# Kernel tuning notes

Hardware: AMD Instinct MI355X
Metric: run time of the kernel (lower is better)

## Reference

```python
import jax, jax.numpy as jnp
import numpy as np

V, D, N, E, H = 80000, 300, 32, 64, 4
C = D // H          # per-head out channels (concat -> D)
B, T, U, L = 32, 35, 1024, 3
VG = 50000          # last_idx_globals - last_idx_senses
NEG_SLOPE = 0.2


def setup_inputs() -> dict:
    key = jax.random.key(0)
    ks = jax.random.split(key, 16)
    s = 0.02
    inp = {
        'x_indices': jax.random.randint(ks[0], (B, T, N), 0, V),
        'edge_index': jax.random.randint(ks[1], (B, T, 2, E), 0, N),
        'X': jax.random.normal(ks[2], (V, D), jnp.float32) * s,
        'gat_W': jax.random.normal(ks[3], (D, H * C), jnp.float32) * s,
        'att_src': jax.random.normal(ks[4], (H, C), jnp.float32) * s,
        'att_dst': jax.random.normal(ks[5], (H, C), jnp.float32) * s,
        'gat_bias': jnp.zeros((H * C,), jnp.float32),
        'W_ih0': jax.random.normal(ks[6], (4 * U, 2 * D), jnp.float32) * s,
        'W_ih_rest': jax.random.normal(ks[7], (L - 1, 4 * U, U), jnp.float32) * s,
        'W_hh': jax.random.normal(ks[8], (L, 4 * U, U), jnp.float32) * s,
        'b_ih': jnp.zeros((L, 4 * U), jnp.float32),
        'b_hh': jnp.zeros((L, 4 * U), jnp.float32),
        'lin_W': jax.random.normal(ks[9], (VG, U), jnp.float32) * s,
        'lin_b': jnp.zeros((VG,), jnp.float32),
    }
    return inp


def _gat_node0(X, x_indices, edge_index, gat_W, att_src, att_dst, gat_bias):
    # Batched GATConv over G = B*T tiny subgraphs of fixed size N; dense NxN
    # attention per subgraph is used since N=32 (G*H*N*N ~ 4.6M floats).
    b, t, n = x_indices.shape
    G = b * t
    idx = x_indices.reshape(G, n)
    ei = edge_index.reshape(G, 2, -1)
    x = X[idx]                                   # [G,N,D] embedding gather
    h = (x @ gat_W).reshape(G, n, H, C)          # [G,N,H,C]
    a_s = jnp.einsum('gnhc,hc->gnh', h, att_src)
    a_d = jnp.einsum('gnhc,hc->gnh', h, att_dst)
    # e[g,h,i,j] = leaky_relu(a_dst_i + a_src_j)  (messages j -> i)
    e = a_d.transpose(0, 2, 1)[:, :, :, None] + a_s.transpose(0, 2, 1)[:, :, None, :]
    e = jax.nn.leaky_relu(e, NEG_SLOPE)
    src, dst = ei[:, 0], ei[:, 1]
    g_ar = jnp.arange(G)[:, None]
    adj = jnp.zeros((G, n, n), bool).at[g_ar, dst, src].set(True)
    diag = jnp.arange(n)
    adj = adj.at[:, diag, diag].set(True)        # PyG GATConv adds self-loops
    e = jnp.where(adj[:, None, :, :], e, jnp.float32(-1e9))
    alpha = jax.nn.softmax(e, axis=-1)           # softmax over source nodes j
    out = jnp.einsum('ghij,gjhc->gihc', alpha, h)
    node0 = out[:, 0].reshape(G, H * C) + gat_bias  # only node 0 is consumed
    return node0.reshape(b, t, H * C)


def _lstm_layer(xs, Wi, Wh, bi, bh):
    # xs: [T,B,in]; PyTorch gate order i,f,g,o
    bsz, u = xs.shape[1], Wh.shape[1]
    def step(carry, xt):
        hp, cp = carry
        g = xt @ Wi.T + hp @ Wh.T + (bi + bh)
        i_, f_, gg, o_ = jnp.split(g, 4, axis=-1)
        c = jax.nn.sigmoid(f_) * cp + jax.nn.sigmoid(i_) * jnp.tanh(gg)
        hh = jax.nn.sigmoid(o_) * jnp.tanh(c)
        return (hh, c), hh
    init = (jnp.zeros((bsz, u), xs.dtype), jnp.zeros((bsz, u), xs.dtype))
    _, ys = jax.lax.scan(step, init, xs)
    return ys


def reference(x_indices, edge_index, X, gat_W, att_src, att_dst, gat_bias,
              W_ih0, W_ih_rest, W_hh, b_ih, b_hh, lin_W, lin_b):
    b, t, n = x_indices.shape
    node0 = _gat_node0(X, x_indices, edge_index, gat_W, att_src, att_dst, gat_bias)
    curr_emb = X[x_indices[:, :, 0]]                       # [B,T,D]
    sig = jnp.concatenate([curr_emb, node0], axis=-1)      # [B,T,2D]
    seq = sig.transpose(1, 0, 2)                           # [T,B,2D]
    ys = _lstm_layer(seq, W_ih0, W_hh[0], b_ih[0], b_hh[0])
    for l in range(W_ih_rest.shape[0]):
        ys = _lstm_layer(ys, W_ih_rest[l], W_hh[l + 1], b_ih[l + 1], b_hh[l + 1])
    lstm_out = ys.transpose(1, 0, 2).reshape(b * t, -1)    # [B*T,U]
    logits = lstm_out @ lin_W.T + lin_b                    # [B*T,VG]
    return jax.nn.log_softmax(logits, axis=-1)
```

## Files before the change

### kernel.cpp

```cpp
#include <hip/hip_runtime.h>

#define DEV __device__ __forceinline__

typedef __attribute__((ext_vector_type(8))) short short8;
typedef __attribute__((ext_vector_type(4))) float f32x4;
typedef unsigned short u16;

constexpr int kV = 80000, kD = 300, kNN = 32, kEE = 64, kHH = 4, kCC = 75;
constexpr int kB = 32, kT = 35, kU = 1024, kVG = 50000;
constexpr int kG = kB * kT;
constexpr int kM = kG;

constexpr size_t alignup(size_t x) { return (x + 255) & ~size_t(255); }
constexpr size_t OFF_BAR   = 0;
constexpr size_t OFF_WSRC  = 1024;
constexpr size_t OFF_WDST  = alignup(OFF_WSRC + 1200 * 4);
constexpr size_t OFF_BIAS  = alignup(OFF_WDST + 1200 * 4);
constexpr size_t OFF_SIG   = alignup(OFF_BIAS + 3 * 4096 * 4);
constexpr size_t OFF_WX0   = alignup(OFF_SIG + (size_t)35 * 32 * 640 * 2);
constexpr size_t OFF_WX12  = alignup(OFF_WX0 + (size_t)4096 * 640 * 2);
constexpr size_t OFF_GATES = alignup(OFF_WX12 + (size_t)2 * 4096 * 1024 * 2);
constexpr size_t OFF_HIST  = alignup(OFF_GATES + (size_t)1120 * 4096 * 4);
constexpr size_t OFF_PART  = alignup(OFF_HIST + (size_t)3 * 35 * 32 * 1024 * 2);
constexpr size_t OFF_LSE   = alignup(OFF_PART + (size_t)1120 * 784 * 8);
constexpr size_t OFF_LINWB = alignup(OFF_LSE + 1120 * 4);
constexpr size_t kLinWBytes = (size_t)kVG * 1024 * 2;
constexpr size_t kNeedBW   = OFF_LINWB + kLinWBytes;

DEV u16 f2bf(float f) {
  union { float f; unsigned u; } v; v.f = f;
  unsigned r = v.u + 0x7fffu + ((v.u >> 16) & 1u);
  return (u16)(r >> 16);
}
DEV float fexp(float x) { return __builtin_amdgcn_exp2f(x * 1.4426950408889634f); }
DEV float fsigm(float x) {
  float t = __builtin_amdgcn_exp2f(-1.4426950408889634f * x);
  return __builtin_amdgcn_rcpf(1.f + t);
}
DEV float ftanh(float x) {
  float xc = fminf(fmaxf(x, -20.f), 20.f);
  float t = __builtin_amdgcn_exp2f(2.8853900817779268f * xc);
  return (t - 1.f) * __builtin_amdgcn_rcpf(t + 1.f);
}
DEV f32x4 mfma16(short8 a, short8 b, f32x4 c) {
  return __builtin_amdgcn_mfma_f32_16x16x32_bf16(a, b, c, 0, 0, 0);
}
DEV void store_u16_llc(u16* p, u16 v) {
  unsigned vv = v;
  asm volatile("global_store_short %0, %1, off sc0 sc1"
               :: "v"(p), "v"(vv) : "memory");
}
DEV void gll16(const void* g, void* l) {
  __builtin_amdgcn_global_load_lds(
      (const __attribute__((address_space(1))) unsigned int*)g,
      (__attribute__((address_space(3))) unsigned int*)l, 16, 0, 0);
}
DEV short8 ld8bf(const float* p) {
  float4 a = *(const float4*)p;
  float4 b = *(const float4*)(p + 4);
  u16 t[8] = {f2bf(a.x), f2bf(a.y), f2bf(a.z), f2bf(a.w),
              f2bf(b.x), f2bf(b.y), f2bf(b.z), f2bf(b.w)};
  return *(const short8*)t;
}

__global__ void prep_small(const float* __restrict__ gat_W,
                           const float* __restrict__ att_src,
                           const float* __restrict__ att_dst,
                           const float* __restrict__ b_ih,
                           const float* __restrict__ b_hh,
                           float* __restrict__ ws_src, float* __restrict__ ws_dst,
                           float* __restrict__ bias_sum) {
  int total = 1200 + 1200 + 3 * 4096;
  for (int i = blockIdx.x * blockDim.x + threadIdx.x; i < total; i += gridDim.x * blockDim.x) {
    if (i < 1200) {
      int d = i >> 2, h = i & 3;
      float s = 0.f;
      for (int c = 0; c < kCC; ++c) s += gat_W[d * 300 + h * kCC + c] * att_src[h * kCC + c];
      ws_src[i] = s;
    } else if (i < 2400) {
      int j = i - 1200; int d = j >> 2, h = j & 3;
      float s = 0.f;
      for (int c = 0; c < kCC; ++c) s += gat_W[d * 300 + h * kCC + c] * att_dst[h * kCC + c];
      ws_dst[j] = s;
    } else {
      int j = i - 2400;
      bias_sum[j] = b_ih[j] + b_hh[j];
    }
  }
}

__global__ void wx_prep(const float* __restrict__ W_ih0, u16* __restrict__ wx0) {
  const int n0 = 4096 * 640;
  for (int i = blockIdx.x * blockDim.x + threadIdx.x; i < n0; i += gridDim.x * blockDim.x) {
    int row = i / 640, col = i - row * 640;
    float v = (col < 600) ? W_ih0[row * 600 + col] : 0.f;
    wx0[i] = f2bf(v);
  }
}

__global__ void wb_conv(const float* __restrict__ W, u16* __restrict__ Wb) {
  const long n = (long)kVG * 1024;
  long stride = (long)gridDim.x * blockDim.x * 8;
  for (long i = (long)(blockIdx.x * blockDim.x + threadIdx.x) * 8; i < n; i += stride) {
    float4 a = *(const float4*)(W + i);
    float4 b = *(const float4*)(W + i + 4);
    u16 t[8] = {f2bf(a.x), f2bf(a.y), f2bf(a.z), f2bf(a.w),
                f2bf(b.x), f2bf(b.y), f2bf(b.z), f2bf(b.w)};
    *(uint4*)(Wb + i) = *(const uint4*)t;
  }
}

__global__ void __launch_bounds__(256) gat_kernel(
    const int* __restrict__ x_indices, const int* __restrict__ edge_index,
    const float* __restrict__ X, const float* __restrict__ gat_W,
    const float* __restrict__ gat_bias, const float* __restrict__ ws_src,
    const float* __restrict__ ws_dst, u16* __restrict__ sig) {
  __shared__ float xs[32][301];
  __shared__ float a_s[32][4];
  __shared__ float a_d0[4];
  __shared__ float alpha[4][32];
  __shared__ float xw[4][301];
  __shared__ int allowed[32];
  int g = blockIdx.x, tid = threadIdx.x;
  const int* idx = x_indices + g * 32;
  for (int i = tid; i < 32 * 300; i += 256) {
    int j = i / 300, d2 = i - j * 300;
    xs[j][d2] = X[(size_t)idx[j] * 300 + d2];
  }
  if (tid < 32) allowed[tid] = (tid == 0) ? 1 : 0;
  __syncthreads();
  if (tid < 128) {
    int j = tid >> 2, h = tid & 3;
    float s = 0.f;
    for (int d2 = 0; d2 < 300; ++d2) s += xs[j][d2] * ws_src[d2 * 4 + h];
    a_s[j][h] = s;
  } else if (tid < 132) {
    int h = tid - 128; float s = 0.f;
    for (int d2 = 0; d2 < 300; ++d2) s += xs[0][d2] * ws_dst[d2 * 4 + h];
    a_d0[h] = s;
  } else if (tid >= 192) {
    int e = tid - 192;
    int src = edge_index[g * 128 + e];
    int dst = edge_index[g * 128 + 64 + e];
    if (dst == 0) allowed[src] = 1;
  }
  __syncthreads();
  if (tid < 4) {
    int h = tid;
    float ev[32];
    float mx = -1e30f;
    #pragma unroll
    for (int j = 0; j < 32; ++j) {
      float v = a_d0[h] + a_s[j][h];
      v = (v > 0.f) ? v : 0.2f * v;
      v = allowed[j] ? v : -1e9f;
      ev[j] = v; mx = fmaxf(mx, v);
    }
    float ssum = 0.f;
    #pragma unroll
    for (int j = 0; j < 32; ++j) { float p = fexp(ev[j] - mx); ev[j] = p; ssum += p; }
    float inv = 1.f / ssum;
    #pragma unroll
    for (int j = 0; j < 32; ++j) alpha[h][j] = ev[j] * inv;
  }
  __syncthreads();
  for (int i = tid; i < 4 * 300; i += 256) {
    int h = i / 300, d2 = i - h * 300;
    float s = 0.f;
    #pragma unroll
    for (int j = 0; j < 32; ++j) s += alpha[h][j] * xs[j][d2];
    xw[h][d2] = s;
  }
  __syncthreads();
  int t = g % 35, b = g / 35;
  u16* srow = sig + ((size_t)t * 32 + b) * 640;
  for (int hc = tid; hc < 300; hc += 256) {
    srow[hc] = f2bf(xs[0][hc]);
    int h = hc / 75;
    float s = gat_bias[hc];
    for (int d2 = 0; d2 < 300; ++d2) s += xw[h][d2] * gat_W[d2 * 300 + hc];
    srow[300 + hc] = f2bf(s);
  }
  for (int i2 = 600 + tid; i2 < 640; i2 += 256) srow[i2] = 0;
}

__global__ void __launch_bounds__(256, 4) gemm_ig(
    const u16* __restrict__ A, const u16* __restrict__ Bw,
    float* __restrict__ gates, int K) {
  int bid = blockIdx.x;
  int bm = bid % 9, bn = bid / 9;
  int m0 = bm * 128, n0 = bn * 128;
  int tid = threadIdx.x, w = tid >> 6, lane = tid & 63, l15 = lane & 15, lhi = lane >> 4;
  int wm = w & 1, wn = w >> 1;
  __shared__ u16 As[2][128][32];
  __shared__ u16 Bs[2][128][32];
  int cl = ((lane & 3) ^ ((lane >> 3) & 3)) * 8;
  int am0 = m0 + w * 32 + (lane >> 2);
  int am1 = am0 + 16;
  const u16* arow0 = A + (size_t)((am0 < kM) ? am0 : 0) * K + cl;
  const u16* arow1 = A + (size_t)((am1 < kM) ? am1 : 0) * K + cl;
  int bn0r = n0 + w * 32 + (lane >> 2);
  const u16* brow0 = Bw + (size_t)bn0r * K + cl;
  const u16* brow1 = Bw + (size_t)(bn0r + 16) * K + cl;
  const int koff = (lhi ^ ((l15 >> 1) & 3)) * 8;

  f32x4 acc[4][4];
  #pragma unroll
  for (int i = 0; i < 4; ++i)
    #pragma unroll
    for (int j = 0; j < 4; ++j) { f32x4 z = {0.f, 0.f, 0.f, 0.f}; acc[i][j] = z; }

  auto ISSUE = [&](int k0, int buf) {
    gll16(arow0 + k0, &As[buf][w * 32][0]);
    gll16(arow1 + k0, &As[buf][w * 32 + 16][0]);
    gll16(brow0 + k0, &Bs[buf][w * 32][0]);
    gll16(brow1 + k0, &Bs[buf][w * 32 + 16][0]);
  };
  int nkt = K >> 5;
  ISSUE(0, 0);
  for (int kt = 0; kt < nkt; ++kt) {
    int cur = kt & 1;
    if (kt < nkt - 1) {
      ISSUE((kt + 1) * 32, cur ^ 1);
      asm volatile("s_waitcnt vmcnt(4)" ::: "memory");
    } else {
      asm volatile("s_waitcnt vmcnt(0)" ::: "memory");
    }
    __builtin_amdgcn_s_barrier();
    __builtin_amdgcn_sched_barrier(0);
    short8 bfr[4];
    #pragma unroll
    for (int nt = 0; nt < 4; ++nt)
      bfr[nt] = *(const short8*)&Bs[cur][wn * 64 + nt * 16 + l15][koff];
    #pragma unroll
    for (int mt = 0; mt < 4; ++mt) {
      short8 af = *(const short8*)&As[cur][wm * 64 + mt * 16 + l15][koff];
      #pragma unroll
      for (int nt = 0; nt < 4; ++nt)
        acc[mt][nt] = mfma16(af, bfr[nt], acc[mt][nt]);
    }
    __builtin_amdgcn_sched_barrier(0);
    __builtin_amdgcn_s_barrier();
  }
  #pragma unroll
  for (int mt = 0; mt < 4; ++mt) {
    #pragma unroll
    for (int r = 0; r < 4; ++r) {
      int m = m0 + wm * 64 + mt * 16 + lhi * 4 + r;
      if (m < kM) {
        float* orow = gates + (size_t)m * 4096;
        #pragma unroll
        for (int nt = 0; nt < 4; ++nt) {
          int n = n0 + wn * 64 + nt * 16 + l15;
          orow[(n & 1023) * 4 + (n >> 10)] = acc[mt][nt][r];
        }
      }
    }
  }
}

__global__ void __launch_bounds__(256, 1) lstm_fused012(
    const float* __restrict__ W_hh,
    const float* __restrict__ W_ih_rest,
    const float* __restrict__ gates,
    const float* __restrict__ bias_sum,
    u16* __restrict__ hist0, u16* __restrict__ hist1, u16* __restrict__ hist2,
    unsigned* __restrict__ flags) {
  const int p = blockIdx.x;
  const int u0 = p * 4;
  const int tid = threadIdx.x;
  const int w = tid >> 6, lane = tid & 63, l15 = lane & 15, lhi = lane >> 4;
  __shared__ float pred0[4][16][33];
  __shared__ float pred1[4][16][33];
  __shared__ float pred2[4][16][33];

  const int kbase = w * 256;
  const int grow = (l15 >> 2) * 1024 + u0 + (l15 & 3);
  size_t rowoff = (size_t)grow * 1024 + kbase + lhi * 8;
  const float* pw0 = W_hh + rowoff;
  const float* pw1 = W_hh + (size_t)4096 * 1024 + rowoff;
  const float* pw2 = W_hh + (size_t)2 * 4096 * 1024 + rowoff;
  const float* pi1 = W_ih_rest + rowoff;
  const float* pi2 = W_ih_rest + (size_t)4096 * 1024 + rowoff;
  short8 rw0[8], rw1[8], rw2[8], ri1[8], ri2[8];
  #pragma unroll
  for (int kk = 0; kk < 8; ++kk) {
    rw0[kk] = ld8bf(pw0 + kk * 32);
    rw1[kk] = ld8bf(pw1 + kk * 32);
    rw2[kk] = ld8bf(pw2 + kk * 32);
    ri1[kk] = ld8bf(pi1 + kk * 32);
    ri2[kk] = ld8bf(pi2 + kk * 32);
  }

  const int layerA = tid >> 7;
  const int pbA = (tid & 127) >> 2, pjA = tid & 3;
  float biasA[4], biasB[4];
  #pragma unroll
  for (int g = 0; g < 4; ++g) {
    biasA[g] = bias_sum[layerA * 4096 + g * 1024 + u0 + pjA];
    biasB[g] = bias_sum[2 * 4096 + g * 1024 + u0 + pjA];
  }
  float cA = 0.f, cB = 0.f;
  const unsigned* myflag = flags + w * 64 + lane;
  __syncthreads();

  for (int s = 0; s < 37; ++s) {
    if (s >= 1) {
      unsigned tgt = (unsigned)s;
      while (!__all((int)(__hip_atomic_load(myflag, __ATOMIC_RELAXED,
                                            __HIP_MEMORY_SCOPE_AGENT) >= tgt)))
        __builtin_amdgcn_s_sleep(1);
      asm volatile("" ::: "memory");
    }
    f32x4 a00 = {0,0,0,0}, a01 = {0,0,0,0};
    f32x4 a10 = {0,0,0,0}, a11 = {0,0,0,0};
    f32x4 a20 = {0,0,0,0}, a21 = {0,0,0,0};
    const bool useH0 = (s >= 1 && s <= 35);
    const bool l0h   = (s >= 1 && s < 35);
    const bool useH1 = (s >= 2 && s <= 36);
    const bool l1h   = (s >= 2 && s <= 35);
    const bool useH2 = (s >= 3 && s <= 36);
    if (useH0) {
      const u16* hp = hist0 + (size_t)(s - 1) * 32 * 1024;
      const u16* b0p = hp + l15 * 1024 + lhi * 8 + kbase;
      const u16* b1p = hp + (l15 + 16) * 1024 + lhi * 8 + kbase;
      #pragma unroll
      for (int kk = 0; kk < 8; ++kk) {
        short8 b0 = *(const short8*)(b0p + kk * 32);
        short8 b1 = *(const short8*)(b1p + kk * 32);
        if (l0h) { a00 = mfma16(rw0[kk], b0, a00); a01 = mfma16(rw0[kk], b1, a01); }
        a10 = mfma16(ri1[kk], b0, a10);
        a11 = mfma16(ri1[kk], b1, a11);
      }
    }
    if (useH1) {
      const u16* hp = hist1 + (size_t)(s - 2) * 32 * 1024;
      const u16* c0p = hp + l15 * 1024 + lhi * 8 + kbase;
      const u16* c1p = hp + (l15 + 16) * 1024 + lhi * 8 + kbase;
      #pragma unroll
      for (int kk = 0; kk < 8; ++kk) {
        short8 c0 = *(const short8*)(c0p + kk * 32);
        short8 c1 = *(const short8*)(c1p + kk * 32);
        if (l1h) { a10 = mfma16(rw1[kk], c0, a10); a11 = mfma16(rw1[kk], c1, a11); }
        a20 = mfma16(ri2[kk], c0, a20);
        a21 = mfma16(ri2[kk], c1, a21);
      }
    }
    if (useH2) {
      const u16* hp = hist2 + (size_t)(s - 3) * 32 * 1024;
      const u16* d0p = hp + l15 * 1024 + lhi * 8 + kbase;
      const u16* d1p = hp + (l15 + 16) * 1024 + lhi * 8 + kbase;
      #pragma unroll
      for (int kk = 0; kk < 8; ++kk) {
        short8 d0 = *(const short8*)(d0p + kk * 32);
        short8 d1 = *(const short8*)(d1p + kk * 32);
        a20 = mfma16(rw2[kk], d0, a20);
        a21 = mfma16(rw2[kk], d1, a21);
      }
    }
    #pragma unroll
    for (int r = 0; r < 4; ++r) {
      pred0[w][lhi * 4 + r][l15]      = a00[r];
      pred0[w][lhi * 4 + r][l15 + 16] = a01[r];
      pred1[w][lhi * 4 + r][l15]      = a10[r];
      pred1[w][lhi * 4 + r][l15 + 16] = a11[r];
      pred2[w][lhi * 4 + r][l15]      = a20[r];
      pred2[w][lhi * 4 + r][l15 + 16] = a21[r];
    }
    __syncthreads();
    const bool actA = (layerA == 0) ? (s < 35) : (s >= 1 && s <= 35);
    if (actA) {
      int row = 0;
      float pre[4];
      if (layerA == 0) {
        #pragma unroll
        for (int g = 0; g < 4; ++g) {
          row = g * 4 + pjA;
          pre[g] = pred0[0][row][pbA] + pred0[1][row][pbA] +
                   pred0[2][row][pbA] + pred0[3][row][pbA];
        }
        float4 gx = ((const float4*)gates)[(size_t)(s * 32 + pbA) * 1024 + u0 + pjA];
        pre[0] += gx.x; pre[1] += gx.y; pre[2] += gx.z; pre[3] += gx.w;
      } else {
        #pragma unroll
        for (int g = 0; g < 4; ++g) {
          row = g * 4 + pjA;
          pre[g] = pred1[0][row][pbA] + pred1[1][row][pbA] +
                   pred1[2][row][pbA] + pred1[3][row][pbA];
        }
      }
      float iv = pre[0] + biasA[0];
      float fv = pre[1] + biasA[1];
      float gv = pre[2] + biasA[2];
      float ov = pre[3] + biasA[3];
      float cc = fsigm(fv) * cA + fsigm(iv) * ftanh(gv);
      float hh = fsigm(ov) * ftanh(cc);
      cA = cc;
      int t = (layerA == 0) ? s : (s - 1);
      u16* dst = (layerA == 0) ? hist0 : hist1;
      store_u16_llc(dst + ((size_t)(t * 32 + pbA) << 10) + u0 + pjA, f2bf(hh));
    }
    if (tid < 128 && s >= 2) {
      float pre[4];
      #pragma unroll
      for (int g = 0; g < 4; ++g) {
        int row = g * 4 + pjA;
        pre[g] = pred2[0][row][pbA] + pred2[1][row][pbA] +
                 pred2[2][row][pbA] + pred2[3][row][pbA];
      }
      float iv = pre[0] + biasB[0];
      float fv = pre[1] + biasB[1];
      float gv = pre[2] + biasB[2];
      float ov = pre[3] + biasB[3];
      float cc = fsigm(fv) * cB + fsigm(iv) * ftanh(gv);
      float hh = fsigm(ov) * ftanh(cc);
      cB = cc;
      int t = s - 2;
      store_u16_llc(hist2 + ((size_t)(t * 32 + pbA) << 10) + u0 + pjA, f2bf(hh));
    }
    __syncthreads();
    if (s < 36 && tid == 0)
      __hip_atomic_store(flags + p, (unsigned)(s + 1),
                         __ATOMIC_RELAXED, __HIP_MEMORY_SCOPE_AGENT);
  }
}

DEV void logits_epilogue(f32x4 (&acc)[4][4], int m0, int n0, int wm, int wn,
                         int l15, int lhi, const float* lin_b,
                         float* out, float2* partials, int bn) {
  float bcol[4]; int ncol[4];
  #pragma unroll
  for (int nt = 0; nt < 4; ++nt) {
    int n = n0 + wn * 64 + nt * 16 + l15;
    ncol[nt] = n;
    bcol[nt] = (n < kVG) ? lin_b[n] : -INFINITY;
  }
  #pragma unroll
  for (int mt = 0; mt < 4; ++mt) {
    #pragma unroll
    for (int r = 0; r < 4; ++r) {
      int m = m0 + wm * 64 + mt * 16 + lhi * 4 + r;
      float v0 = acc[mt][0][r] + bcol[0];
      float v1 = acc[mt][1][r] + bcol[1];
      float v2 = acc[mt][2][r] + bcol[2];
      float v3 = acc[mt][3][r] + bcol[3];
      bool mok = (m < kM);
      if (mok) {
        float* orow = out + (size_t)m * kVG;
        if (ncol[0] < kVG) orow[ncol[0]] = v0;
        if (ncol[1] < kVG) orow[ncol[1]] = v1;
        if (ncol[2] < kVG) orow[ncol[2]] = v2;
        if (ncol[3] < kVG) orow[ncol[3]] = v3;
      }
      float mx = fmaxf(fmaxf(v0, v1), fmaxf(v2, v3));
      #pragma unroll
      for (int d2 = 1; d2 < 16; d2 <<= 1) mx = fmaxf(mx, __shfl_xor(mx, d2, 64));
      float sv = 0.f;
      sv += (v0 > -1e30f) ? fexp(v0 - mx) : 0.f;
      sv += (v1 > -1e30f) ? fexp(v1 - mx) : 0.f;
      sv += (v2 > -1e30f) ? fexp(v2 - mx) : 0.f;
      sv += (v3 > -1e30f) ? fexp(v3 - mx) : 0.f;
      #pragma unroll
      for (int d2 = 1; d2 < 16; d2 <<= 1) sv += __shfl_xor(sv, d2, 64);
      if (mok && l15 == 0)
        partials[(size_t)m * 784 + bn * 2 + wn] = make_float2(mx, sv);
    }
  }
}

__global__ void __launch_bounds__(256, 4) gemm_logits_async(
    const u16* __restrict__ hist2, const u16* __restrict__ linwb,
    const float* __restrict__ lin_b, float* __restrict__ out,
    float2* __restrict__ partials) {
  int nwg = gridDim.x, orig = blockIdx.x;
  int q = nwg >> 3, r = nwg & 7, xcd = orig & 7, off = orig >> 3;
  int bid = (xcd < r ? xcd * (q + 1) : r * (q + 1) + (xcd - r) * q) + off;
  int bm = bid % 9, bn = bid / 9;
  int m0 = bm * 128, n0 = bn * 128;
  int tid = threadIdx.x, w = tid >> 6, lane = tid & 63, l15 = lane & 15, lhi = lane >> 4;
  int wm = w & 1, wn = w >> 1;
  __shared__ u16 As[2][128][32];
  __shared__ u16 Bs[2][128][32];
  int cl = ((lane & 3) ^ ((lane >> 3) & 3)) * 8;
  int am0 = m0 + w * 32 + (lane >> 2);
  int am1 = am0 + 16;
  int mm0 = (am0 < kM) ? am0 : 0, mm1 = (am1 < kM) ? am1 : 0;
  const u16* arow0 = hist2 + (((size_t)((mm0 % 35) * 32 + mm0 / 35)) << 10) + cl;
  const u16* arow1 = hist2 + (((size_t)((mm1 % 35) * 32 + mm1 / 35)) << 10) + cl;
  int nr0 = n0 + w * 32 + (lane >> 2);
  int nn0 = (nr0 < kVG) ? nr0 : 0, nn1 = (nr0 + 16 < kVG) ? nr0 + 16 : 0;
  const u16* brow0 = linwb + ((size_t)nn0 << 10) + cl;
  const u16* brow1 = linwb + ((size_t)nn1 << 10) + cl;
  const int koff = (lhi ^ ((l15 >> 1) & 3)) * 8;

  f32x4 acc[4][4];
  #pragma unroll
  for (int i = 0; i < 4; ++i)
    #pragma unroll
    for (int j = 0; j < 4; ++j) { f32x4 z = {0.f, 0.f, 0.f, 0.f}; acc[i][j] = z; }

  auto ISSUE = [&](int k0, int buf) {
    gll16(arow0 + k0, &As[buf][w * 32][0]);
    gll16(arow1 + k0, &As[buf][w * 32 + 16][0]);
    gll16(brow0 + k0, &Bs[buf][w * 32][0]);
    gll16(brow1 + k0, &Bs[buf][w * 32 + 16][0]);
  };
  ISSUE(0, 0);
  for (int kt = 0; kt < 32; ++kt) {
    int cur = kt & 1;
    if (kt < 31) {
      ISSUE((kt + 1) * 32, cur ^ 1);
      asm volatile("s_waitcnt vmcnt(4)" ::: "memory");
    } else {
      asm volatile("s_waitcnt vmcnt(0)" ::: "memory");
    }
    __builtin_amdgcn_s_barrier();
    __builtin_amdgcn_sched_barrier(0);
    short8 bfr[4];
    #pragma unroll
    for (int nt = 0; nt < 4; ++nt)
      bfr[nt] = *(const short8*)&Bs[cur][wn * 64 + nt * 16 + l15][koff];
    #pragma unroll
    for (int mt = 0; mt < 4; ++mt) {
      short8 af = *(const short8*)&As[cur][wm * 64 + mt * 16 + l15][koff];
      #pragma unroll
      for (int nt = 0; nt < 4; ++nt)
        acc[mt][nt] = mfma16(af, bfr[nt], acc[mt][nt]);
    }
    __builtin_amdgcn_sched_barrier(0);
    __builtin_amdgcn_s_barrier();
  }
  logits_epilogue(acc, m0, n0, wm, wn, l15, lhi, lin_b, out, partials, bn);
}

__global__ void __launch_bounds__(256, 1) gemm_logits_fb(
    const u16* __restrict__ hist2, const float* __restrict__ lin_W,
    const float* __restrict__ lin_b, float* __restrict__ out,
    float2* __restrict__ partials) {
  int nwg = gridDim.x, orig = blockIdx.x;
  int q = nwg >> 3, r = nwg & 7, xcd = orig & 7, off = orig >> 3;
  int bid = (xcd < r ? xcd * (q + 1) : r * (q + 1) + (xcd - r) * q) + off;
  int bm = bid % 9, bn = bid / 9;
  int m0 = bm * 128, n0 = bn * 128;
  int tid = threadIdx.x, w = tid >> 6, lane = tid & 63, l15 = lane & 15, lhi = lane >> 4;
  int wm = w & 1, wn = w >> 1;
  __shared__ u16 As[128][40];
  __shared__ u16 Bs[128][40];
  f32x4 acc[4][4];
  #pragma unroll
  for (int i = 0; i < 4; ++i)
    #pragma unroll
    for (int j = 0; j < 4; ++j) { f32x4 z = {0.f, 0.f, 0.f, 0.f}; acc[i][j] = z; }
  for (int kt = 0; kt < 32; ++kt) {
    int k0 = kt * 32;
    #pragma unroll
    for (int q2 = 0; q2 < 2; ++q2) {
      int c = tid * 2 + q2; int row = c >> 2; int ch = c & 3;
      int m = m0 + row;
      uint4 av{0u, 0u, 0u, 0u};
      if (m < kM) {
        int b = m / 35; int t = m - b * 35;
        av = *(const uint4*)(hist2 + ((size_t)(t * 32 + b) << 10) + k0 + ch * 8);
      }
      *(uint4*)&As[row][ch * 8] = av;
      int n = n0 + row;
      uint4 bv{0u, 0u, 0u, 0u};
      if (n < kVG) {
        const float* src = lin_W + (size_t)n * 1024 + k0 + ch * 8;
        float4 f0 = *(const float4*)(src);
        float4 f1 = *(const float4*)(src + 4);
        bv.x = (unsigned)f2bf(f0.x) | ((unsigned)f2bf(f0.y) << 16);
        bv.y = (unsigned)f2bf(f0.z) | ((unsigned)f2bf(f0.w) << 16);
        bv.z = (unsigned)f2bf(f1.x) | ((unsigned)f2bf(f1.y) << 16);
        bv.w = (unsigned)f2bf(f1.z) | ((unsigned)f2bf(f1.w) << 16);
      }
      *(uint4*)&Bs[row][ch * 8] = bv;
    }
    __syncthreads();
    short8 bfr[4];
    #pragma unroll
    for (int nt = 0; nt < 4; ++nt)
      bfr[nt] = *(const short8*)&Bs[wn * 64 + nt * 16 + l15][lhi * 8];
    #pragma unroll
    for (int mt = 0; mt < 4; ++mt) {
      short8 af = *(const short8*)&As[wm * 64 + mt * 16 + l15][lhi * 8];
      #pragma unroll
      for (int nt = 0; nt < 4; ++nt)
        acc[mt][nt] = mfma16(af, bfr[nt], acc[mt][nt]);
    }
    __syncthreads();
  }
  logits_epilogue(acc, m0, n0, wm, wn, l15, lhi, lin_b, out, partials, bn);
}

__global__ void reduce_rows(const float2* __restrict__ partials, float* __restrict__ lse) {
  int m = blockIdx.x, tid = threadIdx.x;
  float mx = -INFINITY, s = 0.f;
  for (int j = tid; j < 782; j += 256) {
    float2 p = partials[(size_t)m * 784 + j];
    if (p.x > mx) { s = s * fexp(mx - p.x) + p.y; mx = p.x; }
    else          { s += p.y * fexp(p.x - mx); }
  }
  for (int d = 1; d < 64; d <<= 1) {
    float omx = __shfl_xor(mx, d, 64);
    float os  = __shfl_xor(s, d, 64);
    if (omx > mx) { s = s * fexp(mx - omx) + os; mx = omx; }
    else          { s += os * fexp(omx - mx); }
  }
  __shared__ float smx[4], ssum[4];
  int w = tid >> 6;
  if ((tid & 63) == 0) { smx[w] = mx; ssum[w] = s; }
  __syncthreads();
  if (tid == 0) {
    for (int i = 1; i < 4; ++i) {
      float omx = smx[i], os = ssum[i];
      if (omx > mx) { s = s * fexp(mx - omx) + os; mx = omx; }
      else          { s += os * fexp(omx - mx); }
    }
    lse[m] = mx + logf(s);
  }
}

__global__ void sub_lse(float* __restrict__ out, const float* __restrict__ lse) {
  const int total4 = 14000000;
  for (int i = blockIdx.x * blockDim.x + threadIdx.x; i < total4; i += gridDim.x * blockDim.x) {
    int m = i / 12500;
    float4 v = ((float4*)out)[i];
    float L = lse[m];
    v.x -= L; v.y -= L; v.z -= L; v.w -= L;
    ((float4*)out)[i] = v;
  }
}

extern "C" void kernel_launch(void* const* d_in, const int* in_sizes, int n_in,
                              void* d_out, int out_size, void* d_ws, size_t ws_size,
                              hipStream_t stream) {
  const int*   x_indices  = (const int*)d_in[0];
  const int*   edge_index = (const int*)d_in[1];
  const float* X          = (const float*)d_in[2];
  const float* gat_W      = (const float*)d_in[3];
  const float* att_src    = (const float*)d_in[4];
  const float* att_dst    = (const float*)d_in[5];
  const float* gat_bias   = (const float*)d_in[6];
  const float* W_ih0      = (const float*)d_in[7];
  const float* W_ih_rest  = (const float*)d_in[8];
  const float* W_hh       = (const float*)d_in[9];
  const float* b_ih       = (const float*)d_in[10];
  const float* b_hh       = (const float*)d_in[11];
  const float* lin_W      = (const float*)d_in[12];
  const float* lin_b      = (const float*)d_in[13];
  float* out = (float*)d_out;
  char* ws = (char*)d_ws;

  unsigned* flags    = (unsigned*)(ws + OFF_BAR);
  float*    ws_src   = (float*)(ws + OFF_WSRC);
  float*    ws_dst   = (float*)(ws + OFF_WDST);
  float*    bias_sum = (float*)(ws + OFF_BIAS);
  u16*      sig      = (u16*)(ws + OFF_SIG);
  u16*      wx0      = (u16*)(ws + OFF_WX0);
  float*    gates    = (float*)(ws + OFF_GATES);
  u16*      hist     = (u16*)(ws + OFF_HIST);
  float2*   partials = (float2*)(ws + OFF_PART);
  float*    lse      = (float*)(ws + OFF_LSE);
  u16*      linwb    = (u16*)(ws + OFF_LINWB);
  bool use_bw = (ws_size >= kNeedBW);

  u16* hist0 = hist;
  u16* hist1 = hist + (size_t)35 * 32 * 1024;
  u16* hist2 = hist + (size_t)2 * 35 * 32 * 1024;

  hipMemsetAsync(ws + OFF_BAR, 0, 1024, stream);
  prep_small<<<64, 256, 0, stream>>>(gat_W, att_src, att_dst, b_ih, b_hh,
                                     ws_src, ws_dst, bias_sum);
  wx_prep<<<512, 256, 0, stream>>>(W_ih0, wx0);
  if (use_bw) wb_conv<<<2048, 256, 0, stream>>>(lin_W, linwb);
  gat_kernel<<<kG, 256, 0, stream>>>(x_indices, edge_index, X, gat_W, gat_bias,
                                     ws_src, ws_dst, sig);
  gemm_ig<<<288, 256, 0, stream>>>(sig, wx0, gates, 640);
  lstm_fused012<<<256, 256, 0, stream>>>(W_hh, W_ih_rest, gates, bias_sum,
                                         hist0, hist1, hist2, flags);
  if (use_bw)
    gemm_logits_async<<<9 * 391, 256, 0, stream>>>(hist2, linwb, lin_b, out, partials);
  else
    gemm_logits_fb<<<9 * 391, 256, 0, stream>>>(hist2, lin_W, lin_b, out, partials);
  reduce_rows<<<kG, 256, 0, stream>>>(partials, lse);
  sub_lse<<<2048, 256, 0, stream>>>(out, lse);
}
```

Baseline: 909.7 us.

## Split persistent LSTM work across 8 waves by matrix job and K-half

The fused 3-layer wavefront LSTM kernel moves from 256 to 512 threads per block. Each wave now owns one weight-matrix job (W_hh0, W_ih1, W_hh1+W_ih2, W_hh2) over half of K, instead of every wave doing all five matrices over a quarter of K. Each wave waits only on the flags for the history it reads. This shortens the per-step serial MFMA chain and spreads register-resident weights over more waves, at the cost of load imbalance (job 2 does double work), more waves per block contending, and 16-deep weight arrays per wave.

Result: faster. 889.9 us (-2.2%).

```diff
diff --git a/kernel.cpp b/kernel.cpp
--- a/kernel.cpp
+++ b/kernel.cpp
@@ -259,7 +259,7 @@
   }
 }
 
-__global__ void __launch_bounds__(256, 1) lstm_fused012(
+__global__ void __launch_bounds__(512, 1) lstm_fused012(
     const float* __restrict__ W_hh,
     const float* __restrict__ W_ih_rest,
     const float* __restrict__ gates,
@@ -270,153 +270,133 @@
   const int u0 = p * 4;
   const int tid = threadIdx.x;
   const int w = tid >> 6, lane = tid & 63, l15 = lane & 15, lhi = lane >> 4;
-  __shared__ float pred0[4][16][33];
+  const int khalf = w & 1;
+  const int job = w >> 1;
+  const int kbase = khalf * 512;
+  __shared__ float pred0[2][16][33];
   __shared__ float pred1[4][16][33];
   __shared__ float pred2[4][16][33];
 
-  const int kbase = w * 256;
   const int grow = (l15 >> 2) * 1024 + u0 + (l15 & 3);
   size_t rowoff = (size_t)grow * 1024 + kbase + lhi * 8;
-  const float* pw0 = W_hh + rowoff;
-  const float* pw1 = W_hh + (size_t)4096 * 1024 + rowoff;
-  const float* pw2 = W_hh + (size_t)2 * 4096 * 1024 + rowoff;
-  const float* pi1 = W_ih_rest + rowoff;
-  const float* pi2 = W_ih_rest + (size_t)4096 * 1024 + rowoff;
-  short8 rw0[8], rw1[8], rw2[8], ri1[8], ri2[8];
+  const float* m1;
+  const float* m2 = W_ih_rest + (size_t)4096 * 1024 + rowoff;
+  if (job == 0)      m1 = W_hh + rowoff;
+  else if (job == 1) m1 = W_ih_rest + rowoff;
+  else if (job == 2) m1 = W_hh + (size_t)4096 * 1024 + rowoff;
+  else               m1 = W_hh + (size_t)2 * 4096 * 1024 + rowoff;
+  short8 r1[16], r2[16];
   #pragma unroll
-  for (int kk = 0; kk < 8; ++kk) {
-    rw0[kk] = ld8bf(pw0 + kk * 32);
-    rw1[kk] = ld8bf(pw1 + kk * 32);
-    rw2[kk] = ld8bf(pw2 + kk * 32);
-    ri1[kk] = ld8bf(pi1 + kk * 32);
-    ri2[kk] = ld8bf(pi2 + kk * 32);
-  }
-
-  const int layerA = tid >> 7;
-  const int pbA = (tid & 127) >> 2, pjA = tid & 3;
-  float biasA[4], biasB[4];
-  #pragma unroll
-  for (int g = 0; g < 4; ++g) {
-    biasA[g] = bias_sum[layerA * 4096 + g * 1024 + u0 + pjA];
-    biasB[g] = bias_sum[2 * 4096 + g * 1024 + u0 + pjA];
-  }
-  float cA = 0.f, cB = 0.f;
-  const unsigned* myflag = flags + w * 64 + lane;
+  for (int kk = 0; kk < 16; ++kk) r1[kk] = ld8bf(m1 + kk * 32);
+  if (job == 2) {
+    #pragma unroll
+    for (int kk = 0; kk < 16; ++kk) r2[kk] = ld8bf(m2 + kk * 32);
+  }
+
+  const int pw_layer = tid >> 7;
+  const int pb = (tid & 127) >> 2, pj = tid & 3;
+  float bias_r[4] = {0.f, 0.f, 0.f, 0.f};
+  if (pw_layer < 3) {
+    #pragma unroll
+    for (int g = 0; g < 4; ++g)
+      bias_r[g] = bias_sum[pw_layer * 4096 + g * 1024 + u0 + pj];
+  }
+  float c_reg = 0.f;
+  const unsigned* f0p = flags + khalf * 128 + lane;
   __syncthreads();
 
   for (int s = 0; s < 37; ++s) {
-    if (s >= 1) {
+    bool active; const u16* hsrc;
+    if (job == 0)      { active = (s >= 1 && s < 35);  hsrc = hist0 + (size_t)(s - 1) * 32 * 1024; }
+    else if (job == 1) { active = (s >= 1 && s <= 35); hsrc = hist0 + (size_t)(s - 1) * 32 * 1024; }
+    else if (job == 2) { active = (s >= 2 && s <= 36); hsrc = hist1 + (size_t)(s - 2) * 32 * 1024; }
+    else               { active = (s >= 3 && s <= 36); hsrc = hist2 + (size_t)(s - 3) * 32 * 1024; }
+    if (active) {
       unsigned tgt = (unsigned)s;
-      while (!__all((int)(__hip_atomic_load(myflag, __ATOMIC_RELAXED,
-                                            __HIP_MEMORY_SCOPE_AGENT) >= tgt)))
+      while (!__all((int)((__hip_atomic_load(f0p, __ATOMIC_RELAXED,
+                                             __HIP_MEMORY_SCOPE_AGENT) >= tgt) &
+                          (__hip_atomic_load(f0p + 64, __ATOMIC_RELAXED,
+                                             __HIP_MEMORY_SCOPE_AGENT) >= tgt))))
         __builtin_amdgcn_s_sleep(1);
       asm volatile("" ::: "memory");
     }
-    f32x4 a00 = {0,0,0,0}, a01 = {0,0,0,0};
-    f32x4 a10 = {0,0,0,0}, a11 = {0,0,0,0};
-    f32x4 a20 = {0,0,0,0}, a21 = {0,0,0,0};
-    const bool useH0 = (s >= 1 && s <= 35);
-    const bool l0h   = (s >= 1 && s < 35);
-    const bool useH1 = (s >= 2 && s <= 36);
-    const bool l1h   = (s >= 2 && s <= 35);
-    const bool useH2 = (s >= 3 && s <= 36);
-    if (useH0) {
-      const u16* hp = hist0 + (size_t)(s - 1) * 32 * 1024;
-      const u16* b0p = hp + l15 * 1024 + lhi * 8 + kbase;
-      const u16* b1p = hp + (l15 + 16) * 1024 + lhi * 8 + kbase;
-      #pragma unroll
-      for (int kk = 0; kk < 8; ++kk) {
-        short8 b0 = *(const short8*)(b0p + kk * 32);
-        short8 b1 = *(const short8*)(b1p + kk * 32);
-        if (l0h) { a00 = mfma16(rw0[kk], b0, a00); a01 = mfma16(rw0[kk], b1, a01); }
-        a10 = mfma16(ri1[kk], b0, a10);
-        a11 = mfma16(ri1[kk], b1, a11);
+    f32x4 a0 = {0,0,0,0}, a1 = {0,0,0,0}, a2 = {0,0,0,0}, a3 = {0,0,0,0};
+    if (active) {
+      const u16* b0p = hsrc + l15 * 1024 + kbase + lhi * 8;
+      const u16* b1p = hsrc + (l15 + 16) * 1024 + kbase + lhi * 8;
+      if (job == 2) {
+        #pragma unroll
+        for (int kk = 0; kk < 16; ++kk) {
+          short8 b0 = *(const short8*)(b0p + kk * 32);
+          short8 b1 = *(const short8*)(b1p + kk * 32);
+          a0 = mfma16(r1[kk], b0, a0);
+          a1 = mfma16(r1[kk], b1, a1);
+          a2 = mfma16(r2[kk], b0, a2);
+          a3 = mfma16(r2[kk], b1, a3);
+        }
+      } else {
+        #pragma unroll
+        for (int kk = 0; kk < 16; ++kk) {
+          short8 b0 = *(const short8*)(b0p + kk * 32);
+          short8 b1 = *(const short8*)(b1p + kk * 32);
+          a0 = mfma16(r1[kk], b0, a0);
+          a1 = mfma16(r1[kk], b1, a1);
+        }
       }
     }
-    if (useH1) {
-      const u16* hp = hist1 + (size_t)(s - 2) * 32 * 1024;
-      const u16* c0p = hp + l15 * 1024 + lhi * 8 + kbase;
-      const u16* c1p = hp + (l15 + 16) * 1024 + lhi * 8 + kbase;
-      #pragma unroll
-      for (int kk = 0; kk < 8; ++kk) {
-        short8 c0 = *(const short8*)(c0p + kk * 32);
-        short8 c1 = *(const short8*)(c1p + kk * 32);
-        if (l1h) { a10 = mfma16(rw1[kk], c0, a10); a11 = mfma16(rw1[kk], c1, a11); }
-        a20 = mfma16(ri2[kk], c0, a20);
-        a21 = mfma16(ri2[kk], c1, a21);
+    #pragma unroll
+    for (int r = 0; r < 4; ++r) {
+      int row = lhi * 4 + r;
+      if (job == 0) {
+        pred0[khalf][row][l15] = a0[r];      pred0[khalf][row][l15 + 16] = a1[r];
+      } else if (job == 1) {
+        pred1[khalf][row][l15] = a0[r];      pred1[khalf][row][l15 + 16] = a1[r];
+      } else if (job == 2) {
+        pred1[2 + khalf][row][l15] = a0[r];  pred1[2 + khalf][row][l15 + 16] = a1[r];
+        pred2[khalf][row][l15] = a2[r];      pred2[khalf][row][l15 + 16] = a3[r];
+      } else {
+        pred2[2 + khalf][row][l15] = a0[r];  pred2[2 + khalf][row][l15 + 16] = a1[r];
       }
     }
-    if (useH2) {
-      const u16* hp = hist2 + (size_t)(s - 3) * 32 * 1024;
-      const u16* d0p = hp + l15 * 1024 + lhi * 8 + kbase;
-      const u16* d1p = hp + (l15 + 16) * 1024 + lhi * 8 + kbase;
-      #pragma unroll
-      for (int kk = 0; kk < 8; ++kk) {
-        short8 d0 = *(const short8*)(d0p + kk * 32);
-        short8 d1 = *(const short8*)(d1p + kk * 32);
-        a20 = mfma16(rw2[kk], d0, a20);
-        a21 = mfma16(rw2[kk], d1, a21);
-      }
-    }
-    #pragma unroll
-    for (int r = 0; r < 4; ++r) {
-      pred0[w][lhi * 4 + r][l15]      = a00[r];
-      pred0[w][lhi * 4 + r][l15 + 16] = a01[r];
-      pred1[w][lhi * 4 + r][l15]      = a10[r];
-      pred1[w][lhi * 4 + r][l15 + 16] = a11[r];
-      pred2[w][lhi * 4 + r][l15]      = a20[r];
-      pred2[w][lhi * 4 + r][l15 + 16] = a21[r];
-    }
     __syncthreads();
-    const bool actA = (layerA == 0) ? (s < 35) : (s >= 1 && s <= 35);
-    if (actA) {
-      int row = 0;
+    bool act = (pw_layer == 0) ? (s < 35)
+             : (pw_layer == 1) ? (s >= 1 && s <= 35)
+             : (pw_layer == 2) ? (s >= 2 && s <= 36) : false;
+    if (act) {
       float pre[4];
-      if (layerA == 0) {
+      if (pw_layer == 0) {
         #pragma unroll
         for (int g = 0; g < 4; ++g) {
-          row = g * 4 + pjA;
-          pre[g] = pred0[0][row][pbA] + pred0[1][row][pbA] +
-                   pred0[2][row][pbA] + pred0[3][row][pbA];
+          int row = g * 4 + pj;
+          pre[g] = pred0[0][row][pb] + pred0[1][row][pb];
         }
-        float4 gx = ((const float4*)gates)[(size_t)(s * 32 + pbA) * 1024 + u0 + pjA];
+        float4 gx = ((const float4*)gates)[(size_t)(s * 32 + pb) * 1024 + u0 + pj];
         pre[0] += gx.x; pre[1] += gx.y; pre[2] += gx.z; pre[3] += gx.w;
+      } else if (pw_layer == 1) {
+        #pragma unroll
+        for (int g = 0; g < 4; ++g) {
+          int row = g * 4 + pj;
+          pre[g] = pred1[0][row][pb] + pred1[1][row][pb] +
+                   pred1[2][row][pb] + pred1[3][row][pb];
+        }
       } else {
         #pragma unroll
         for (int g = 0; g < 4; ++g) {
-          row = g * 4 + pjA;
-          pre[g] = pred1[0][row][pbA] + pred1[1][row][pbA] +
-                   pred1[2][row][pbA] + pred1[3][row][pbA];
+          int row = g * 4 + pj;
+          pre[g] = pred2[0][row][pb] + pred2[1][row][pb] +
+                   pred2[2][row][pb] + pred2[3][row][pb];
         }
       }
-      float iv = pre[0] + biasA[0];
-      float fv = pre[1] + biasA[1];
-      float gv = pre[2] + biasA[2];
-      float ov = pre[3] + biasA[3];
-      float cc = fsigm(fv) * cA + fsigm(iv) * ftanh(gv);
+      float iv = pre[0] + bias_r[0];
+      float fv = pre[1] + bias_r[1];
+      float gv = pre[2] + bias_r[2];
+      float ov = pre[3] + bias_r[3];
+      float cc = fsigm(fv) * c_reg + fsigm(iv) * ftanh(gv);
       float hh = fsigm(ov) * ftanh(cc);
-      cA = cc;
-      int t = (layerA == 0) ? s : (s - 1);
-      u16* dst = (layerA == 0) ? hist0 : hist1;
-      store_u16_llc(dst + ((size_t)(t * 32 + pbA) << 10) + u0 + pjA, f2bf(hh));
-    }
-    if (tid < 128 && s >= 2) {
-      float pre[4];
-      #pragma unroll
-      for (int g = 0; g < 4; ++g) {
-        int row = g * 4 + pjA;
-        pre[g] = pred2[0][row][pbA] + pred2[1][row][pbA] +
-                 pred2[2][row][pbA] + pred2[3][row][pbA];
-      }
-      float iv = pre[0] + biasB[0];
-      float fv = pre[1] + biasB[1];
-      float gv = pre[2] + biasB[2];
-      float ov = pre[3] + biasB[3];
-      float cc = fsigm(fv) * cB + fsigm(iv) * ftanh(gv);
-      float hh = fsigm(ov) * ftanh(cc);
-      cB = cc;
-      int t = s - 2;
-      store_u16_llc(hist2 + ((size_t)(t * 32 + pbA) << 10) + u0 + pjA, f2bf(hh));
+      c_reg = cc;
+      int t = s - pw_layer;
+      u16* dst = (pw_layer == 0) ? hist0 : (pw_layer == 1) ? hist1 : hist2;
+      store_u16_llc(dst + ((size_t)(t * 32 + pb) << 10) + u0 + pj, f2bf(hh));
     }
     __syncthreads();
     if (s < 36 && tid == 0)
@@ -677,7 +657,7 @@
   gat_kernel<<<kG, 256, 0, stream>>>(x_indices, edge_index, X, gat_W, gat_bias,
                                      ws_src, ws_dst, sig);
   gemm_ig<<<288, 256, 0, stream>>>(sig, wx0, gates, 640);
-  lstm_fused012<<<256, 256, 0, stream>>>(W_hh, W_ih_rest, gates, bias_sum,
+  lstm_fused012<<<256, 512, 0, stream>>>(W_hh, W_ih_rest, gates, bias_sum,
                                          hist0, hist1, hist2, flags);
   if (use_bw)
     gemm_logits_async<<<9 * 391, 256, 0, stream>>>(hist2, linwb, lin_b, out, partials);
```
